# Performance work log

Hardware: AMD Instinct MI355X
Metric: run time of the kernel (lower is better)

Reference implementation:

```python
import jax, jax.numpy as jnp
import numpy as np

N_STREAMS = 4
SINKHORN_ITERS = 20
EPS = 1e-8


def sinkhorn_knopp(log_mat, num_iters=SINKHORN_ITERS, eps=EPS):
    mat = jnp.exp(log_mat)
    def body(_, m):
        m = m / (m.sum(axis=-2, keepdims=True) + eps)
        m = m / (m.sum(axis=-1, keepdims=True) + eps)
        return m
    return jax.lax.fori_loop(0, num_iters, body, mat)


def setup_inputs() -> dict:
    key = jax.random.key(0)
    B, L, C = 4, 2048, 1024
    n = N_STREAMS
    hidden = 4 * C
    ks = jax.random.split(key, 8)
    def xavier(k, shape):
        fan_in, fan_out = shape[0], shape[1]
        lim = np.sqrt(6.0 / (fan_in + fan_out))
        return jax.random.uniform(k, shape, jnp.float32, -lim, lim)
    return {
        "x": jax.random.normal(ks[0], (B, L, C), jnp.float32),
        "rms_weight": jnp.ones((C * n,), jnp.float32),
        "W_dyn": xavier(ks[1], (C * n, n * n + 2 * n)),  # Linear no-bias, stored [in,out]
        "bias_pre": jnp.zeros((1, n), jnp.float32),
        "bias_post": jnp.zeros((1, n), jnp.float32),
        "bias_res": jnp.zeros((n, n), jnp.float32),
        "alpha_pre": jnp.full((1,), 0.01, jnp.float32),
        "alpha_post": jnp.full((1,), 0.01, jnp.float32),
        "alpha_res": jnp.full((1,), 0.01, jnp.float32),
        "W1": xavier(ks[2], (C, hidden)),
        "b1": jnp.zeros((hidden,), jnp.float32),
        "W2": xavier(ks[3], (hidden, C)),
        "b2": jnp.zeros((C,), jnp.float32),
        "Wout": xavier(ks[4], (C * n, C)),
        "bout": jnp.zeros((C,), jnp.float32),
    }


def reference(x, rms_weight, W_dyn, bias_pre, bias_post, bias_res,
              alpha_pre, alpha_post, alpha_res, W1, b1, W2, b2, Wout, bout):
    B, L, C = x.shape
    n = bias_pre.shape[1]
    # x expanded across streams (broadcast view, no copy)
    x_exp = jnp.broadcast_to(x[:, :, None, :], (B, L, n, C))  # [B,L,n,C]
    x_flat = x_exp.reshape(B, L, n * C)
    # RMSNorm
    rms = jnp.sqrt(jnp.mean(x_flat * x_flat, axis=-1, keepdims=True) + EPS)
    x_norm = x_flat / rms * rms_weight
    # dynamic projection
    dynamic = x_norm @ W_dyn  # [B,L,n*n+2n]
    dyn_pre = dynamic[..., :n]
    dyn_post = dynamic[..., n:2 * n]
    dyn_res = dynamic[..., 2 * n:].reshape(B, L, n, n)
    H_pre = jax.nn.sigmoid(alpha_pre * dyn_pre + bias_pre)            # [B,L,n]
    H_post = 2.0 * jax.nn.sigmoid(alpha_post * dyn_post + bias_post)  # [B,L,n]
    H_res = sinkhorn_knopp(alpha_res * dyn_res + bias_res)            # [B,L,n,n]
    # pre-mix streams then residual MLP
    pre_mixed = jnp.einsum('bln,blnc->blc', H_pre, x_exp)
    h = jax.nn.gelu(pre_mixed @ W1 + b1, approximate=False)
    f_out = h @ W2 + b2  # [B,L,C]
    # post mixing + doubly-stochastic residual mixing
    post_mixed = H_post[..., None] * f_out[:, :, None, :]             # [B,L,n,C]
    res_mixed = jnp.einsum('blnm,blmc->blnc', H_res, x_exp)
    merged = (res_mixed + post_mixed).reshape(B, L, n * C)
    return merged @ Wout + bout + x
```

## Files before the change

### kernel.cpp

```cpp
#include <hip/hip_runtime.h>

typedef unsigned short u16;
typedef __bf16 bf16x8 __attribute__((ext_vector_type(8)));
typedef float f32x4 __attribute__((ext_vector_type(4)));

__device__ __forceinline__ u16 f2bf(float f) {
  unsigned int u = __builtin_bit_cast(unsigned int, f);
  u += 0x7fffu + ((u >> 16) & 1u);
  return (u16)(u >> 16);
}

__device__ __forceinline__ void gload_lds16(const u16* g, u16* l) {
  __builtin_amdgcn_global_load_lds((const __attribute__((address_space(1))) unsigned int*)g,
                                   (__attribute__((address_space(3))) unsigned int*)l,
                                   16, 0, 0);
}

__device__ __forceinline__ float gelu_erf(float v) {
  const float z = v * 0.70710678118654752f;
  const float az = fabsf(z);
  const float t = __builtin_amdgcn_rcpf(1.0f + 0.3275911f * az);
  const float p = t * (0.254829592f +
                  t * (-0.284496736f +
                  t * (1.421413741f +
                  t * (-1.453152027f + t * 1.061405429f))));
  const float e = __expf(-az * az);
  float er = 1.0f - p * e;
  er = (z < 0.f) ? -er : er;
  return 0.5f * v * (1.0f + er);
}


__global__ __launch_bounds__(256) void weff_kernel(const float* __restrict__ rmsw,
                                                   const float* __restrict__ Wdyn,
                                                   float* __restrict__ WT) {
  int idx = blockIdx.x * 256 + threadIdx.x;
  int j = idx >> 10, c = idx & 1023;
  float s = 0.f;
#pragma unroll
  for (int st = 0; st < 4; ++st) {
    int r = st * 1024 + c;
    s += rmsw[r] * Wdyn[(long)r * 24 + j];
  }
  WT[idx] = s;
}

__global__ __launch_bounds__(256) void pack_all(const float* __restrict__ W1,
                                                const float* __restrict__ W2,
                                                const float* __restrict__ WO,
                                                u16* __restrict__ F1,
                                                u16* __restrict__ F2,
                                                u16* __restrict__ FO) {
  const int blk = blockIdx.x;
  const int sel = blk >> 11;
  const float* W;
  u16* FMB;
  int lgN, KC;
  if (sel == 0)      { W = W1; FMB = F1; lgN = 12; KC = 32; }
  else if (sel == 1) { W = W2; FMB = F2; lgN = 10; KC = 128; }
  else               { W = WO; FMB = FO; lgN = 10; KC = 128; }
  const long gid = (long)(blk & 2047) * 256 + threadIdx.x;
  const int N = 1 << lgN;
  const int n = (int)(gid & (N - 1));
  const int k0 = (int)(gid >> lgN) * 8;
  unsigned int p[4];
#pragma unroll
  for (int d = 0; d < 4; ++d) {
    const float lo = W[(long)(k0 + 2 * d) * N + n];
    const float hi = W[(long)(k0 + 2 * d + 1) * N + n];
    p[d] = (unsigned)f2bf(lo) | ((unsigned)f2bf(hi) << 16);
  }
  const long ad = ((long)(n >> 4) * KC + (k0 >> 5)) * 512 +
                  ((n & 15) + (((k0 >> 3) & 3) << 4)) * 8;
  *(uint4*)(FMB + ad) = make_uint4(p[0], p[1], p[2], p[3]);
}

__global__ __launch_bounds__(512) void prep_tokens(
    const float* __restrict__ x, const float* __restrict__ WT,
    const float* __restrict__ bias_pre, const float* __restrict__ bias_post,
    const float* __restrict__ bias_res, const float* __restrict__ a_pre,
    const float* __restrict__ a_post, const float* __restrict__ a_res,
    u16* __restrict__ preA, float* __restrict__ scal) {
  const int tid = threadIdx.x;
  const int b = blockIdx.x;
  const long t0 = (long)b * 16;

  __shared__ float red[32][16][26];
  __shared__ float tot2[16][26];
  __shared__ float spre[16];

  {
    const int tt = tid & 15;
    const int cc = tid >> 4;
    const float* xp = x + (t0 + tt) * 1024 + cc * 32;
    float part[25];
#pragma unroll
    for (int j = 0; j < 25; ++j) part[j] = 0.f;
#pragma unroll
    for (int g = 0; g < 8; ++g) {
      const float4 xv = *(const float4*)(xp + g * 4);
      part[24] += xv.x * xv.x + xv.y * xv.y + xv.z * xv.z + xv.w * xv.w;
#pragma unroll
      for (int j = 0; j < 24; ++j) {
        const float4 wv = *(const float4*)(WT + (long)j * 1024 + cc * 32 + g * 4);
        part[j] += xv.x * wv.x + xv.y * wv.y + xv.z * wv.z + xv.w * wv.w;
      }
    }
#pragma unroll
    for (int j = 0; j < 25; ++j) red[cc][tt][j] = part[j];
  }
  __syncthreads();

  {
    const int tt = tid >> 5;
    const int j = tid & 31;
    if (j < 25) {
      float s = 0.f;
#pragma unroll
      for (int cc = 0; cc < 32; ++cc) s += red[cc][tt][j];
      tot2[tt][j] = s;
    }
  }
  __syncthreads();

  if (tid < 256) {
    const int tt = tid >> 4;
    const int m = tid & 15;
    const long t = t0 + tt;
    const float rms = sqrtf(tot2[tt][24] * (1.0f / 1024.0f) + 1e-8f);
    const float rinv = 1.0f / rms;

    if (m == 0) {
      const float ap = a_pre[0];
      float s_pre = 0.f;
#pragma unroll
      for (int i = 0; i < 4; ++i)
        s_pre += 1.f / (1.f + expf(-(ap * tot2[tt][i] * rinv + bias_pre[i])));
      spre[tt] = s_pre;
    }
    if (m < 4) {
      const float apo = a_post[0];
      float hp = 2.f / (1.f + expf(-(apo * tot2[tt][4 + m] * rinv + bias_post[m])));
      scal[t * 8 + 4 + m] = hp;
    }
    const float ar = a_res[0];
    float Mv = expf(ar * tot2[tt][8 + m] * rinv + bias_res[m]);
#pragma unroll
    for (int it = 0; it < 20; ++it) {
      float cs = Mv + __shfl_xor(Mv, 4);
      cs += __shfl_xor(cs, 8);
      Mv = Mv / (cs + 1e-8f);
      float rs = Mv + __shfl_xor(Mv, 1);
      rs += __shfl_xor(rs, 2);
      Mv = Mv / (rs + 1e-8f);
    }
    float rs = Mv + __shfl_xor(Mv, 1);
    rs += __shfl_xor(rs, 2);
    if ((m & 3) == 0) scal[t * 8 + (m >> 2)] = rs;
  }
  __syncthreads();

  {
    const int w = tid >> 6;
    const int lane = tid & 63;
    const int tl = lane & 15;
    const int co = (lane >> 4) * 8;
    const float sp = spre[tl];
#pragma unroll
    for (int p = 0; p < 4; ++p) {
      const int ki = p * 8 + w;
      const float* xr = x + (t0 + tl) * 1024 + ki * 32 + co;
      const float4 xa = *(const float4*)(xr);
      const float4 xb = *(const float4*)(xr + 4);
      unsigned q0 = (unsigned)f2bf(sp * xa.x) | ((unsigned)f2bf(sp * xa.y) << 16);
      unsigned q1 = (unsigned)f2bf(sp * xa.z) | ((unsigned)f2bf(sp * xa.w) << 16);
      unsigned q2 = (unsigned)f2bf(sp * xb.x) | ((unsigned)f2bf(sp * xb.y) << 16);
      unsigned q3 = (unsigned)f2bf(sp * xb.z) | ((unsigned)f2bf(sp * xb.w) << 16);
      *(uint4*)(preA + ((long)b * 32 + ki) * 512 + lane * 8) = make_uint4(q0, q1, q2, q3);
    }
  }
}

template <int EPI, int NT, int LGGX>
__global__ __launch_bounds__(512, 2) void gemm_fm2(const u16* __restrict__ A,
                                                   const u16* __restrict__ B,
                                                   const int KCtot, const int KCout,
                                                   const float* __restrict__ bias,
                                                   const float* __restrict__ X,
                                                   const float* __restrict__ scal,
                                                   void* __restrict__ dstv) {
  constexpr int CH = 16 + NT;
  constexpr int SC = CH / 8;
  constexpr int AI = (NT == 16) ? 8 : 4;
  const int tid = threadIdx.x;
  const int lane = tid & 63;
  const int wave = tid >> 6;
  const int wm = (NT == 16) ? (wave >> 2) : (wave >> 1);
  const int wn = (NT == 16) ? (wave & 3) : (wave & 1);
  const int b = blockIdx.x;
  const int c = b & 7;
  const int s = b >> 3;
  const int bx = s & ((1 << LGGX) - 1);
  const int by = c * 4 + (s >> LGGX);

  __shared__ u16 lds[4][CH][512];
  u16* const l0 = (u16*)lds;

  const u16* gb[4];
#pragma unroll
  for (int l = 0; l < SC; ++l) {
    const int t = wave * SC + l;
    gb[l] = (t < 16) ? (A + ((long)(by * 16 + t) * KCtot) * 512 + lane * 8)
                     : (B + ((long)(bx * NT + (t - 16)) * KCtot) * 512 + lane * 8);
  }

#define STG(kt)                                                              \
  {                                                                          \
    u16* cb_ = l0 + (((kt) & 3) * CH + wave * SC) * 512;                     \
    const long ko_ = (long)(kt)*512;                                         \
    _Pragma("unroll") for (int l_ = 0; l_ < SC; ++l_)                        \
        gload_lds16(gb[l_] + ko_, cb_ + l_ * 512);                           \
  }

  f32x4 acc[AI][4] = {};

  STG(0); STG(1); STG(2);
  if constexpr (SC == 4) asm volatile("s_waitcnt vmcnt(8)" ::: "memory");
  else                   asm volatile("s_waitcnt vmcnt(6)" ::: "memory");
  __builtin_amdgcn_s_barrier();

  for (int kt = 0; kt < KCtot; ++kt) {
    if (kt + 3 < KCtot) STG(kt + 3);
    const u16* cb = l0 + (kt & 3) * (CH * 512);
    bf16x8 af[AI], bf[4];
#pragma unroll
    for (int i = 0; i < AI; ++i)
      af[i] = *(const bf16x8*)(cb + (wm * AI + i) * 512 + lane * 8);
#pragma unroll
    for (int j = 0; j < 4; ++j)
      bf[j] = *(const bf16x8*)(cb + (16 + wn * 4 + j) * 512 + lane * 8);
    asm volatile("s_waitcnt lgkmcnt(0)" ::: "memory");
    __builtin_amdgcn_sched_barrier(0);
    __builtin_amdgcn_s_setprio(1);
#pragma unroll
    for (int i = 0; i < AI; ++i)
#pragma unroll
      for (int j = 0; j < 4; ++j)
        acc[i][j] = __builtin_amdgcn_mfma_f32_16x16x32_bf16(af[i], bf[j], acc[i][j], 0, 0, 0);
    __builtin_amdgcn_s_setprio(0);
    if (kt + 4 <= KCtot) {
      if constexpr (SC == 4) asm volatile("s_waitcnt vmcnt(8)" ::: "memory");
      else                   asm volatile("s_waitcnt vmcnt(6)" ::: "memory");
    } else if (kt + 3 == KCtot) {
      if constexpr (SC == 4) asm volatile("s_waitcnt vmcnt(4)" ::: "memory");
      else                   asm volatile("s_waitcnt vmcnt(3)" ::: "memory");
    } else {
      asm volatile("s_waitcnt vmcnt(0)" ::: "memory");
    }
    __builtin_amdgcn_s_barrier();
  }
#undef STG

  if constexpr (EPI == 0) {
    u16* dst = (u16*)dstv;
    u16* ep = l0 + wave * 8192;
#pragma unroll
    for (int i = 0; i < AI; ++i)
#pragma unroll
      for (int j = 0; j < 4; ++j) {
        const int col = bx * 256 + wn * 64 + j * 16 + (lane & 15);
        const float bcol = bias[col];
#pragma unroll
        for (int r = 0; r < 4; ++r) {
          const float g = gelu_erf(acc[i][j][r] + bcol);
          const int lp = ((lane >> 4) * 4 + r) | ((((j & 1) << 1) | ((lane & 15) >> 3)) << 4);
          ep[(i * 2 + (j >> 1)) * 512 + lp * 8 + (lane & 7)] = f2bf(g);
        }
      }
#pragma unroll
    for (int ch = 0; ch < 2 * AI; ++ch) {
      const int i = ch >> 1, jc = ch & 1;
      const long row16 = by * 16 + wm * 8 + i;
      const long col32 = bx * 8 + wn * 2 + jc;
      *(uint4*)(dst + (row16 * KCout + col32) * 512 + lane * 8) =
          *(const uint4*)(ep + ch * 512 + lane * 8);
    }
  } else if constexpr (EPI == 1) {
    u16* dst = (u16*)dstv;
    u16* ep = l0 + wave * 4096;
#pragma unroll
    for (int i = 0; i < AI; ++i) {
      float rr[4][4], hh[4][4];
#pragma unroll
      for (int r = 0; r < 4; ++r) {
        const int row = by * 256 + wm * 64 + i * 16 + (lane >> 4) * 4 + r;
        const float4 rv = *(const float4*)(scal + (long)row * 8);
        const float4 hv = *(const float4*)(scal + (long)row * 8 + 4);
        rr[r][0] = rv.x; rr[r][1] = rv.y; rr[r][2] = rv.z; rr[r][3] = rv.w;
        hh[r][0] = hv.x; hh[r][1] = hv.y; hh[r][2] = hv.z; hh[r][3] = hv.w;
      }
#pragma unroll
      for (int jc = 0; jc < 2; ++jc) {
#pragma unroll
        for (int jj = 0; jj < 2; ++jj) {
          const int j = jc * 2 + jj;
          const int col = bx * 128 + wn * 64 + j * 16 + (lane & 15);
          const float bcol = bias[col];
#pragma unroll
          for (int r = 0; r < 4; ++r) {
            const int row = by * 256 + wm * 64 + i * 16 + (lane >> 4) * 4 + r;
            const float f = acc[i][j][r] + bcol;
            const float xval = X[(long)row * 1024 + col];
            const int lp = ((lane >> 4) * 4 + r) | (((jj << 1) | ((lane & 15) >> 3)) << 4);
#pragma unroll
            for (int ss = 0; ss < 4; ++ss)
              ep[ss * 512 + lp * 8 + (lane & 7)] = f2bf(rr[r][ss] * xval + hh[r][ss] * f);
          }
        }
        const long row16 = by * 16 + wm * 4 + i;
        const long col32 = bx * 4 + wn * 2 + jc;
#pragma unroll
        for (int ss = 0; ss < 4; ++ss)
          *(uint4*)(dst + (row16 * 128 + (long)ss * 32 + col32) * 512 + lane * 8) =
              *(const uint4*)(ep + ss * 512 + lane * 8);
      }
    }
  } else {
    float* dst = (float*)dstv;
    float* ep32 = (float*)(l0 + wave * 4096);
#pragma unroll
    for (int half = 0; half < 2; ++half) {
#pragma unroll
      for (int i2 = 0; i2 < 2; ++i2) {
        const int i = half * 2 + i2;
#pragma unroll
        for (int j = 0; j < 4; ++j) {
          const int col = bx * 128 + wn * 64 + j * 16 + (lane & 15);
          const float bcol = bias[col];
#pragma unroll
          for (int r = 0; r < 4; ++r) {
            const long row = by * 256 + wm * 64 + i * 16 + (lane >> 4) * 4 + r;
            ep32[(i2 * 16 + (lane >> 4) * 4 + r) * 64 + j * 16 + (lane & 15)] =
                acc[i][j][r] + bcol + X[row * 1024 + col];
          }
        }
      }
#pragma unroll
      for (int q = 0; q < 8; ++q) {
        const int lr = q * 4 + (lane >> 4);
        const long row = by * 256 + wm * 64 + half * 32 + lr;
        const long col = bx * 128 + wn * 64 + (lane & 15) * 4;
        *(float4*)(dst + row * 1024 + col) =
            *(const float4*)(ep32 + lr * 64 + (lane & 15) * 4);
      }
    }
  }
}

extern "C" void kernel_launch(void* const* d_in, const int* in_sizes, int n_in,
                              void* d_out, int out_size, void* d_ws, size_t ws_size,
                              hipStream_t stream) {
  (void)in_sizes; (void)n_in; (void)out_size; (void)ws_size;
  const float* x = (const float*)d_in[0];
  const float* rmsw = (const float*)d_in[1];
  const float* Wdyn = (const float*)d_in[2];
  const float* bias_pre = (const float*)d_in[3];
  const float* bias_post = (const float*)d_in[4];
  const float* bias_res = (const float*)d_in[5];
  const float* a_pre = (const float*)d_in[6];
  const float* a_post = (const float*)d_in[7];
  const float* a_res = (const float*)d_in[8];
  const float* W1 = (const float*)d_in[9];
  const float* b1 = (const float*)d_in[10];
  const float* W2 = (const float*)d_in[11];
  const float* b2 = (const float*)d_in[12];
  const float* Wout = (const float*)d_in[13];
  const float* bout = (const float*)d_in[14];
  float* out = (float*)d_out;
  char* ws = (char*)d_ws;

  constexpr size_t MB = 1048576;
  u16* W1fm = (u16*)(ws);
  u16* W2fm = (u16*)(ws + 8 * MB);
  u16* WOfm = (u16*)(ws + 16 * MB);
  float* WT = (float*)(ws + 24 * MB);
  float* scal = (float*)(ws + 24 * MB + 98304);
  u16* h = (u16*)(ws + 25 * MB);
  u16* merged = (u16*)(ws + 89 * MB);
  u16* preA = (u16*)(ws + 89 * MB);

  weff_kernel<<<96, 256, 0, stream>>>(rmsw, Wdyn, WT);
  pack_all<<<6144, 256, 0, stream>>>(W1, W2, Wout, W1fm, W2fm, WOfm);
  prep_tokens<<<512, 512, 0, stream>>>(x, WT, bias_pre, bias_post, bias_res,
                                       a_pre, a_post, a_res, preA, scal);
  gemm_fm2<0, 16, 4><<<512, 512, 0, stream>>>(preA, W1fm, 32, 128, b1, nullptr, nullptr, h);
  gemm_fm2<1, 8, 3><<<256, 512, 0, stream>>>(h, W2fm, 128, 128, b2, x, scal, merged);
  gemm_fm2<2, 8, 3><<<256, 512, 0, stream>>>(merged, WOfm, 128, 0, bout, x, nullptr, out);
}
```

Baseline: 420.5 us.

## Stage projection weights in LDS and retile first GEMM with swizzled grid

prep_tokens now copies the 24x1024 effective projection weights into shared memory once per block and reads them from LDS instead of global memory. The reduction buffer reuses that same shared array. The first GEMM switches from 256-wide to 128-wide N tiles, doubling the grid to 1024 blocks, with a new block-index swizzle meant to improve L2 locality. The epilogue indexing is generalized to the tile size. The smaller tiles raise parallelism but lower the per-block arithmetic intensity, and the larger LDS footprint in prep_tokens may reduce its occupancy.

New measurement: 428.0 us. Within noise of the previous version (+1.8%).

```diff
diff --git a/kernel.cpp b/kernel.cpp
--- a/kernel.cpp
+++ b/kernel.cpp
@@ -85,15 +85,22 @@
   const int b = blockIdx.x;
   const long t0 = (long)b * 16;
 
-  __shared__ float red[32][16][26];
+  __shared__ float smem[24 * 1024];
   __shared__ float tot2[16][26];
   __shared__ float spre[16];
 
+#pragma unroll
+  for (int q = 0; q < 12; ++q) {
+    const int o = (q * 512 + tid) * 4;
+    *(float4*)(smem + o) = *(const float4*)(WT + o);
+  }
+  __syncthreads();
+
+  float part[25];
   {
     const int tt = tid & 15;
     const int cc = tid >> 4;
     const float* xp = x + (t0 + tt) * 1024 + cc * 32;
-    float part[25];
 #pragma unroll
     for (int j = 0; j < 25; ++j) part[j] = 0.f;
 #pragma unroll
@@ -102,10 +109,16 @@
       part[24] += xv.x * xv.x + xv.y * xv.y + xv.z * xv.z + xv.w * xv.w;
 #pragma unroll
       for (int j = 0; j < 24; ++j) {
-        const float4 wv = *(const float4*)(WT + (long)j * 1024 + cc * 32 + g * 4);
+        const float4 wv = *(const float4*)(smem + j * 1024 + cc * 32 + g * 4);
         part[j] += xv.x * wv.x + xv.y * wv.y + xv.z * wv.z + xv.w * wv.w;
       }
     }
+  }
+  __syncthreads();
+  float (*red)[16][26] = (float(*)[16][26])smem;
+  {
+    const int tt = tid & 15;
+    const int cc = tid >> 4;
 #pragma unroll
     for (int j = 0; j < 25; ++j) red[cc][tt][j] = part[j];
   }
@@ -181,7 +194,7 @@
   }
 }
 
-template <int EPI, int NT, int LGGX>
+template <int EPI, int NT, int SWZ, int LGGX>
 __global__ __launch_bounds__(512, 2) void gemm_fm2(const u16* __restrict__ A,
                                                    const u16* __restrict__ B,
                                                    const int KCtot, const int KCout,
@@ -198,10 +211,17 @@
   const int wm = (NT == 16) ? (wave >> 2) : (wave >> 1);
   const int wn = (NT == 16) ? (wave & 3) : (wave & 1);
   const int b = blockIdx.x;
-  const int c = b & 7;
-  const int s = b >> 3;
-  const int bx = s & ((1 << LGGX) - 1);
-  const int by = c * 4 + (s >> LGGX);
+  int bx, by;
+  if constexpr (SWZ == 1) {
+    const int c = b & 7, u = b >> 3;
+    const int p = u >> 5, v = u & 31;
+    by = (p * 2 + (c >> 2)) * 4 + (v >> 3);
+    bx = (c & 3) * 8 + (v & 7);
+  } else {
+    const int c = b & 7, s = b >> 3;
+    bx = s & ((1 << LGGX) - 1);
+    by = c * 4 + (s >> LGGX);
+  }
 
   __shared__ u16 lds[4][CH][512];
   u16* const l0 = (u16*)lds;
@@ -263,12 +283,12 @@
 
   if constexpr (EPI == 0) {
     u16* dst = (u16*)dstv;
-    u16* ep = l0 + wave * 8192;
+    u16* ep = l0 + wave * (2 * AI * 512);
 #pragma unroll
     for (int i = 0; i < AI; ++i)
 #pragma unroll
       for (int j = 0; j < 4; ++j) {
-        const int col = bx * 256 + wn * 64 + j * 16 + (lane & 15);
+        const int col = bx * (NT * 16) + wn * 64 + j * 16 + (lane & 15);
         const float bcol = bias[col];
 #pragma unroll
         for (int r = 0; r < 4; ++r) {
@@ -280,8 +300,8 @@
 #pragma unroll
     for (int ch = 0; ch < 2 * AI; ++ch) {
       const int i = ch >> 1, jc = ch & 1;
-      const long row16 = by * 16 + wm * 8 + i;
-      const long col32 = bx * 8 + wn * 2 + jc;
+      const long row16 = by * 16 + wm * AI + i;
+      const long col32 = bx * (NT / 2) + wn * 2 + jc;
       *(uint4*)(dst + (row16 * KCout + col32) * 512 + lane * 8) =
           *(const uint4*)(ep + ch * 512 + lane * 8);
     }
@@ -393,7 +413,7 @@
   pack_all<<<6144, 256, 0, stream>>>(W1, W2, Wout, W1fm, W2fm, WOfm);
   prep_tokens<<<512, 512, 0, stream>>>(x, WT, bias_pre, bias_post, bias_res,
                                        a_pre, a_post, a_res, preA, scal);
-  gemm_fm2<0, 16, 4><<<512, 512, 0, stream>>>(preA, W1fm, 32, 128, b1, nullptr, nullptr, h);
-  gemm_fm2<1, 8, 3><<<256, 512, 0, stream>>>(h, W2fm, 128, 128, b2, x, scal, merged);
-  gemm_fm2<2, 8, 3><<<256, 512, 0, stream>>>(merged, WOfm, 128, 0, bout, x, nullptr, out);
-}
+  gemm_fm2<0, 8, 1, 0><<<1024, 512, 0, stream>>>(preA, W1fm, 32, 128, b1, nullptr, nullptr, h);
+  gemm_fm2<1, 8, 0, 3><<<256, 512, 0, stream>>>(h, W2fm, 128, 128, b2, x, scal, merged);
+  gemm_fm2<2, 8, 0, 3><<<256, 512, 0, stream>>>(merged, WOfm, 128, 0, bout, x, nullptr, out);
+}
```
